# Optimization experiments

Measured on AMD Instinct MI355X. Metric: run time of the kernel, lower is better.

## Reference

```python
import jax, jax.numpy as jnp
import numpy as np

HIDDEN = 512
HEADS = 8
HEAD_DIM = HIDDEN // HEADS
N = 262144
G = 1024
LN_EPS = 1e-5
EPS = 1e-8


def setup_inputs() -> dict:
    key = jax.random.key(0)
    ks = jax.random.split(key, 4)
    x = jax.random.normal(ks[0], (N, HIDDEN), dtype=jnp.float32)
    batch = jnp.sort(jax.random.randint(ks[1], (N,), 0, G, dtype=jnp.int32))
    gamma = jnp.ones((HIDDEN,), jnp.float32)
    beta = jnp.zeros((HIDDEN,), jnp.float32)
    W1 = jax.random.normal(ks[2], (HIDDEN, HIDDEN // 2), dtype=jnp.float32) * (HIDDEN ** -0.5)
    b1 = jnp.zeros((HIDDEN // 2,), jnp.float32)
    W2 = jax.random.normal(ks[3], (HIDDEN // 2, HEADS), dtype=jnp.float32) * ((HIDDEN // 2) ** -0.5)
    b2 = jnp.zeros((HEADS,), jnp.float32)
    return {"x": x, "batch": batch, "gamma": gamma, "beta": beta,
            "W1": W1, "b1": b1, "W2": W2, "b2": b2, "num_graphs": G}


def reference(x, batch, gamma, beta, W1, b1, W2, b2, num_graphs):
    n = x.shape[0]
    # LayerNorm over feature dim
    mu = jnp.mean(x, axis=-1, keepdims=True)
    var = jnp.mean(jnp.square(x - mu), axis=-1, keepdims=True)
    x_norm = (x - mu) * jax.lax.rsqrt(var + LN_EPS) * gamma + beta
    # attention MLP -> per-head logits [N, HEADS]
    h = jax.nn.silu(x_norm @ W1 + b1)
    logits = h @ W2 + b2
    # segment softmax per head (all heads vectorized)
    seg_max = jax.ops.segment_max(logits, batch, num_segments=num_graphs)  # [G, HEADS]
    seg_max = jnp.where(jnp.isfinite(seg_max), seg_max, 0.0)  # guard empty segments
    ex = jnp.exp(logits - seg_max[batch])
    denom = jax.ops.segment_sum(ex, batch, num_segments=num_graphs)  # [G, HEADS]
    denom = jnp.where(denom > 0, denom, 1.0)
    weights = ex / denom[batch]  # [N, HEADS]
    # entropy regularizer
    entropy = -jnp.sum(weights * jnp.log(weights + EPS), axis=0) / num_graphs
    mean_entropy = jnp.mean(entropy)
    # per-head weighted features, flattened back, scatter-sum per graph
    x_split = x.reshape(n, HEADS, HEAD_DIM)
    x_weighted = (x_split * weights[:, :, None]).reshape(n, HIDDEN)
    graph_z = jax.ops.segment_sum(x_weighted, batch, num_segments=num_graphs)  # [G, HIDDEN]
    return graph_z, weights, mean_entropy
```

## Files before the change

kernel.cpp:

```cpp
#include <hip/hip_runtime.h>

#define N_ROWS 262144
#define HID 512
#define HHALF 256
#define HEADS 8
#define GNUM 1024
#define LN_EPS 1e-5f
#define POOL_ROWS 128

typedef __bf16 bf16x8 __attribute__((ext_vector_type(8)));
typedef float f32x4 __attribute__((ext_vector_type(4)));

__global__ void k_prep(const float* __restrict__ W1, __bf16* __restrict__ w1t,
                       float* __restrict__ ent, float* __restrict__ graph_z) {
    int tid = blockIdx.x * 256 + threadIdx.x;
    if (tid == 0) *ent = 0.f;
    ((float4*)graph_z)[tid] = make_float4(0.f, 0.f, 0.f, 0.f);
    if (tid < HID * HHALF) {
        int n = tid >> 9;
        int k = tid & 511;
        w1t[n * HID + k] = (__bf16)W1[k * HHALF + n];
    }
}

__global__ void k_seg(const int* __restrict__ batch, int* __restrict__ seg) {
    int g = blockIdx.x * 256 + threadIdx.x;
    if (g > GNUM) return;
    int lo = 0, hi = N_ROWS;
    while (lo < hi) {
        int mid = (lo + hi) >> 1;
        if (batch[mid] < g) lo = mid + 1; else hi = mid;
    }
    seg[g] = lo;
}

__global__ __launch_bounds__(256) void k_stats(const float* __restrict__ x,
                                               float2* __restrict__ stats) {
    int wid = threadIdx.x >> 6, lane = threadIdx.x & 63;
    int row = blockIdx.x * 4 + wid;
    const float* xr = x + (size_t)row * HID + lane * 8;
    float4 a = *(const float4*)xr;
    float4 b = *(const float4*)(xr + 4);
    float s = a.x + a.y + a.z + a.w + b.x + b.y + b.z + b.w;
    float q = a.x*a.x + a.y*a.y + a.z*a.z + a.w*a.w
            + b.x*b.x + b.y*b.y + b.z*b.z + b.w*b.w;
    #pragma unroll
    for (int m = 1; m < 64; m <<= 1) {
        s += __shfl_xor(s, m);
        q += __shfl_xor(q, m);
    }
    if (lane == 0) {
        float mu = s * (1.f / HID);
        float var = q * (1.f / HID) - mu * mu;
        stats[row] = make_float2(mu, rsqrtf(var + LN_EPS));
    }
}

__device__ inline bf16x8 make_af(const float* xp, const float* gp, const float* bp,
                                 float rstd, float nmr) {
    float4 xa = *(const float4*)xp;
    float4 xb = *(const float4*)(xp + 4);
    float4 ga = *(const float4*)gp;
    float4 gb = *(const float4*)(gp + 4);
    float4 ba = *(const float4*)bp;
    float4 bb = *(const float4*)(bp + 4);
    float xs[8] = {xa.x, xa.y, xa.z, xa.w, xb.x, xb.y, xb.z, xb.w};
    float gs[8] = {ga.x, ga.y, ga.z, ga.w, gb.x, gb.y, gb.z, gb.w};
    float bs[8] = {ba.x, ba.y, ba.z, ba.w, bb.x, bb.y, bb.z, bb.w};
    bf16x8 r;
    #pragma unroll
    for (int j = 0; j < 8; ++j)
        r[j] = (__bf16)fmaf(fmaf(xs[j], rstd, nmr), gs[j], bs[j]);
    return r;
}

__global__ __launch_bounds__(256) void k_gemm(
    const float* __restrict__ x, const float2* __restrict__ stats,
    const float* __restrict__ gamma, const float* __restrict__ beta,
    const __bf16* __restrict__ w1t, const float* __restrict__ b1,
    const float* __restrict__ W2, const float* __restrict__ b2,
    float* __restrict__ logits)
{
    __shared__ __align__(16) __bf16 ldsb[256 * 72];
    const int tid = threadIdx.x;
    const int wid = tid >> 6, lane = tid & 63;
    const int q = lane >> 4, c = lane & 15;
    const int rowbase = blockIdx.x * 64 + wid * 16;

    f32x4 acc[16];
    #pragma unroll
    for (int t = 0; t < 16; ++t) acc[t] = (f32x4)0.f;

    const int arow = rowbase + c;
    float2 st = stats[arow];
    const float rstd = st.y;
    const float nmr = -st.x * st.y;
    const float* xrow = x + (size_t)arow * HID;

    const int nrow = tid >> 3, seg = tid & 7;

    for (int s8 = 0; s8 < 8; ++s8) {
        const int k0 = s8 * 64;
        __syncthreads();
        #pragma unroll
        for (int it = 0; it < 8; ++it) {
            int n = nrow + it * 32;
            *(uint4*)(ldsb + n * 72 + seg * 8) =
                *(const uint4*)(w1t + n * HID + k0 + seg * 8);
        }
        __syncthreads();

        bf16x8 af0 = make_af(xrow + k0 + q * 8, gamma + k0 + q * 8, beta + k0 + q * 8,
                             rstd, nmr);
        bf16x8 af1 = make_af(xrow + k0 + 32 + q * 8, gamma + k0 + 32 + q * 8,
                             beta + k0 + 32 + q * 8, rstd, nmr);
        #pragma unroll
        for (int t = 0; t < 16; ++t) {
            int n = t * 16 + c;
            bf16x8 bf0 = *(const bf16x8*)(ldsb + n * 72 + q * 8);
            bf16x8 bf1 = *(const bf16x8*)(ldsb + n * 72 + 32 + q * 8);
            acc[t] = __builtin_amdgcn_mfma_f32_16x16x32_bf16(af0, bf0, acc[t], 0, 0, 0);
            acc[t] = __builtin_amdgcn_mfma_f32_16x16x32_bf16(af1, bf1, acc[t], 0, 0, 0);
        }
    }

    float lp[4][8];
    #pragma unroll
    for (int r = 0; r < 4; ++r)
        #pragma unroll
        for (int hd = 0; hd < 8; ++hd) lp[r][hd] = 0.f;

    #pragma unroll
    for (int t = 0; t < 16; ++t) {
        int n = t * 16 + c;
        float b1v = b1[n];
        float4 w2a = *(const float4*)(W2 + n * 8);
        float4 w2b = *(const float4*)(W2 + n * 8 + 4);
        #pragma unroll
        for (int r = 0; r < 4; ++r) {
            float v = acc[t][r] + b1v;
            float h = v / (1.f + __expf(-v));
            lp[r][0] = fmaf(h, w2a.x, lp[r][0]);
            lp[r][1] = fmaf(h, w2a.y, lp[r][1]);
            lp[r][2] = fmaf(h, w2a.z, lp[r][2]);
            lp[r][3] = fmaf(h, w2a.w, lp[r][3]);
            lp[r][4] = fmaf(h, w2b.x, lp[r][4]);
            lp[r][5] = fmaf(h, w2b.y, lp[r][5]);
            lp[r][6] = fmaf(h, w2b.z, lp[r][6]);
            lp[r][7] = fmaf(h, w2b.w, lp[r][7]);
        }
    }
    #pragma unroll
    for (int m = 1; m < 16; m <<= 1)
        #pragma unroll
        for (int r = 0; r < 4; ++r)
            #pragma unroll
            for (int hd = 0; hd < 8; ++hd)
                lp[r][hd] += __shfl_xor(lp[r][hd], m);

    if (c == 0) {
        float4 b2a = *(const float4*)b2;
        float4 b2b = *(const float4*)(b2 + 4);
        #pragma unroll
        for (int r = 0; r < 4; ++r) {
            int orow = rowbase + q * 4 + r;
            float4 o0 = {lp[r][0] + b2a.x, lp[r][1] + b2a.y,
                         lp[r][2] + b2a.z, lp[r][3] + b2a.w};
            float4 o1 = {lp[r][4] + b2b.x, lp[r][5] + b2b.y,
                         lp[r][6] + b2b.z, lp[r][7] + b2b.w};
            *(float4*)(logits + (size_t)orow * 8) = o0;
            *(float4*)(logits + (size_t)orow * 8 + 4) = o1;
        }
    }
}

__global__ __launch_bounds__(256) void k_smax(
    const float* __restrict__ logits, const int* __restrict__ seg,
    float* __restrict__ smaxt, float* __restrict__ sinvt)
{
    const int g = blockIdx.x;
    const int tid = threadIdx.x;
    const int s = seg[g], e = seg[g + 1];
    __shared__ float red[4][8];
    __shared__ float smx[8];
    const int wid = tid >> 6, lane = tid & 63;

    if (e <= s) {
        if (tid < 8) { smaxt[g * 8 + tid] = 0.f; sinvt[g * 8 + tid] = 1.f; }
        return;
    }
    float mx[8];
    #pragma unroll
    for (int h = 0; h < 8; ++h) mx[h] = -1e30f;
    for (int i = s + tid; i < e; i += 256) {
        float4 l0 = *(const float4*)(logits + (size_t)i * 8);
        float4 l1 = *(const float4*)(logits + (size_t)i * 8 + 4);
        mx[0] = fmaxf(mx[0], l0.x); mx[1] = fmaxf(mx[1], l0.y);
        mx[2] = fmaxf(mx[2], l0.z); mx[3] = fmaxf(mx[3], l0.w);
        mx[4] = fmaxf(mx[4], l1.x); mx[5] = fmaxf(mx[5], l1.y);
        mx[6] = fmaxf(mx[6], l1.z); mx[7] = fmaxf(mx[7], l1.w);
    }
    #pragma unroll
    for (int m = 1; m < 64; m <<= 1)
        #pragma unroll
        for (int h = 0; h < 8; ++h) mx[h] = fmaxf(mx[h], __shfl_xor(mx[h], m));
    if (lane == 0) {
        #pragma unroll
        for (int h = 0; h < 8; ++h) red[wid][h] = mx[h];
    }
    __syncthreads();
    if (tid < 8)
        smx[tid] = fmaxf(fmaxf(red[0][tid], red[1][tid]),
                         fmaxf(red[2][tid], red[3][tid]));
    __syncthreads();
    float sm[8];
    #pragma unroll
    for (int h = 0; h < 8; ++h) sm[h] = smx[h];
    float su[8] = {0, 0, 0, 0, 0, 0, 0, 0};
    for (int i = s + tid; i < e; i += 256) {
        float4 l0 = *(const float4*)(logits + (size_t)i * 8);
        float4 l1 = *(const float4*)(logits + (size_t)i * 8 + 4);
        su[0] += __expf(l0.x - sm[0]); su[1] += __expf(l0.y - sm[1]);
        su[2] += __expf(l0.z - sm[2]); su[3] += __expf(l0.w - sm[3]);
        su[4] += __expf(l1.x - sm[4]); su[5] += __expf(l1.y - sm[5]);
        su[6] += __expf(l1.z - sm[6]); su[7] += __expf(l1.w - sm[7]);
    }
    #pragma unroll
    for (int m = 1; m < 64; m <<= 1)
        #pragma unroll
        for (int h = 0; h < 8; ++h) su[h] += __shfl_xor(su[h], m);
    if (lane == 0) {
        #pragma unroll
        for (int h = 0; h < 8; ++h) red[wid][h] = su[h];
    }
    __syncthreads();
    if (tid < 8) {
        float d = red[0][tid] + red[1][tid] + red[2][tid] + red[3][tid];
        smaxt[g * 8 + tid] = smx[tid];
        sinvt[g * 8 + tid] = 1.f / (d > 0.f ? d : 1.f);
    }
}

__global__ __launch_bounds__(256) void k_wts(
    const float* __restrict__ logits, const int* __restrict__ batch,
    const float* __restrict__ smaxt, const float* __restrict__ sinvt,
    float* __restrict__ weights, float* __restrict__ ent)
{
    const int tid = threadIdx.x;
    const int i0 = blockIdx.x * 256;
    const int h = tid & 7;
    float e = 0.f;
    #pragma unroll
    for (int it = 0; it < 8; ++it) {
        int i = i0 + (tid >> 3) + it * 32;
        int g = batch[i];
        float l = logits[(size_t)i * 8 + h];
        float w = __expf(l - smaxt[g * 8 + h]) * sinvt[g * 8 + h];
        weights[(size_t)i * 8 + h] = w;
        e += w * __logf(w + 1e-8f);
    }
    #pragma unroll
    for (int m = 1; m < 64; m <<= 1) e += __shfl_xor(e, m);
    __shared__ float red[4];
    if ((tid & 63) == 0) red[tid >> 6] = e;
    __syncthreads();
    if (tid == 0)
        atomicAdd(ent, (red[0] + red[1] + red[2] + red[3]) * (-1.f / (GNUM * 8.f)));
}

__global__ __launch_bounds__(256) void k_pool2(
    const float* __restrict__ x, const int* __restrict__ batch,
    const float* __restrict__ weights, float* __restrict__ graph_z)
{
    const int tid = threadIdx.x;
    const int r0 = blockIdx.x * POOL_ROWS;
    const int h = tid >> 5;
    const int f = tid * 2;
    float a0 = 0.f, a1 = 0.f;
    int gcur = batch[r0];
    const int gend = batch[r0 + POOL_ROWS - 1];

    if (gcur == gend) {
        #pragma unroll 4
        for (int r = 0; r < POOL_ROWS; ++r) {
            const size_t i = (size_t)(r0 + r);
            float2 xv = *(const float2*)(x + i * HID + f);
            float w = weights[i * 8 + h];
            a0 = fmaf(xv.x, w, a0);
            a1 = fmaf(xv.y, w, a1);
        }
        atomicAdd(graph_z + (size_t)gcur * HID + f, a0);
        atomicAdd(graph_z + (size_t)gcur * HID + f + 1, a1);
    } else {
        for (int r = 0; r < POOL_ROWS; ++r) {
            const int i = r0 + r;
            const int g = batch[i];
            if (g != gcur) {
                atomicAdd(graph_z + (size_t)gcur * HID + f, a0);
                atomicAdd(graph_z + (size_t)gcur * HID + f + 1, a1);
                a0 = 0.f; a1 = 0.f; gcur = g;
            }
            float2 xv = *(const float2*)(x + (size_t)i * HID + f);
            float w = weights[(size_t)i * 8 + h];
            a0 = fmaf(xv.x, w, a0);
            a1 = fmaf(xv.y, w, a1);
        }
        atomicAdd(graph_z + (size_t)gcur * HID + f, a0);
        atomicAdd(graph_z + (size_t)gcur * HID + f + 1, a1);
    }
}

extern "C" void kernel_launch(void* const* d_in, const int* in_sizes, int n_in,
                              void* d_out, int out_size, void* d_ws, size_t ws_size,
                              hipStream_t stream)
{
    const float* x     = (const float*)d_in[0];
    const int*   batch = (const int*)d_in[1];
    const float* gamma = (const float*)d_in[2];
    const float* beta  = (const float*)d_in[3];
    const float* W1    = (const float*)d_in[4];
    const float* b1    = (const float*)d_in[5];
    const float* W2    = (const float*)d_in[6];
    const float* b2    = (const float*)d_in[7];

    char* ws = (char*)d_ws;
    float2* stats  = (float2*)ws;
    float*  logits = (float*)(ws + (size_t)2 * 1024 * 1024);
    __bf16* w1t    = (__bf16*)(ws + (size_t)10 * 1024 * 1024);
    int*    seg    = (int*)(ws + (size_t)10 * 1024 * 1024 + 256 * 1024);
    float*  smaxt  = (float*)(ws + (size_t)10 * 1024 * 1024 + 512 * 1024);
    float*  sinvt  = (float*)(ws + (size_t)10 * 1024 * 1024 + 576 * 1024);

    float* out     = (float*)d_out;
    float* graph_z = out;
    float* weights = out + (size_t)GNUM * HID;
    float* ent     = out + (size_t)GNUM * HID + (size_t)N_ROWS * HEADS;

    k_prep <<<512, 256, 0, stream>>>(W1, w1t, ent, graph_z);
    k_seg  <<<5, 256, 0, stream>>>(batch, seg);
    k_stats<<<N_ROWS / 4, 256, 0, stream>>>(x, stats);
    k_gemm <<<N_ROWS / 64, 256, 0, stream>>>(x, stats, gamma, beta, w1t, b1, W2, b2, logits);
    k_smax <<<GNUM, 256, 0, stream>>>(logits, seg, smaxt, sinvt);
    k_wts  <<<N_ROWS / 256, 256, 0, stream>>>(logits, batch, smaxt, sinvt, weights, ent);
    k_pool2<<<N_ROWS / POOL_ROWS, 256, 0, stream>>>(x, batch, weights, graph_z);
}
```

Measured before the change: 1.098 ms.

## Fold LayerNorm into GEMM epilogue and drop separate stats pass

Folds gamma into the bf16 W1 copy and precomputes the column sums gamma·W1 and beta·W1, so the GEMM runs on raw x and applies mean/rstd as a per-row affine correction in the epilogue. Row statistics are now computed inside the GEMM kernel from the x fragments it already loads, which removes the k_stats kernel and its extra full read of x (512 MB). The A fragments for all of K are held in registers (8x2 bf16x8), which raises register pressure and may lower occupancy. Rounding raw x to bf16 before normalization changes numerics slightly, and the column sums use atomics.

```diff
diff --git a/kernel.cpp b/kernel.cpp
--- a/kernel.cpp
+++ b/kernel.cpp
@@ -11,16 +11,34 @@
 typedef __bf16 bf16x8 __attribute__((ext_vector_type(8)));
 typedef float f32x4 __attribute__((ext_vector_type(4)));
 
-__global__ void k_prep(const float* __restrict__ W1, __bf16* __restrict__ w1t,
-                       float* __restrict__ ent, float* __restrict__ graph_z) {
+__global__ void k_prep(const float* __restrict__ W1, const float* __restrict__ gamma,
+                       __bf16* __restrict__ w1t, float* __restrict__ ent,
+                       float* __restrict__ graph_z, float* __restrict__ G1,
+                       float* __restrict__ BB) {
     int tid = blockIdx.x * 256 + threadIdx.x;
     if (tid == 0) *ent = 0.f;
+    if (blockIdx.x == 0) { G1[threadIdx.x] = 0.f; BB[threadIdx.x] = 0.f; }
     ((float4*)graph_z)[tid] = make_float4(0.f, 0.f, 0.f, 0.f);
-    if (tid < HID * HHALF) {
-        int n = tid >> 9;
-        int k = tid & 511;
-        w1t[n * HID + k] = (__bf16)W1[k * HHALF + n];
-    }
+    int n = tid >> 9;
+    int k = tid & 511;
+    w1t[n * HID + k] = (__bf16)(gamma[k] * W1[k * HHALF + n]);
+}
+
+__global__ void k_cols(const float* __restrict__ W1, const float* __restrict__ gamma,
+                       const float* __restrict__ beta, float* __restrict__ G1,
+                       float* __restrict__ BB) {
+    int n = threadIdx.x;
+    int k0 = blockIdx.x * 64;
+    float g = 0.f, b = 0.f;
+    #pragma unroll
+    for (int kk = 0; kk < 64; ++kk) {
+        int k = k0 + kk;
+        float w = W1[(size_t)k * HHALF + n];
+        g = fmaf(gamma[k], w, g);
+        b = fmaf(beta[k], w, b);
+    }
+    atomicAdd(G1 + n, g);
+    atomicAdd(BB + n, b);
 }
 
 __global__ void k_seg(const int* __restrict__ batch, int* __restrict__ seg) {
@@ -34,50 +52,17 @@
     seg[g] = lo;
 }
 
-__global__ __launch_bounds__(256) void k_stats(const float* __restrict__ x,
-                                               float2* __restrict__ stats) {
-    int wid = threadIdx.x >> 6, lane = threadIdx.x & 63;
-    int row = blockIdx.x * 4 + wid;
-    const float* xr = x + (size_t)row * HID + lane * 8;
-    float4 a = *(const float4*)xr;
-    float4 b = *(const float4*)(xr + 4);
-    float s = a.x + a.y + a.z + a.w + b.x + b.y + b.z + b.w;
-    float q = a.x*a.x + a.y*a.y + a.z*a.z + a.w*a.w
-            + b.x*b.x + b.y*b.y + b.z*b.z + b.w*b.w;
-    #pragma unroll
-    for (int m = 1; m < 64; m <<= 1) {
-        s += __shfl_xor(s, m);
-        q += __shfl_xor(q, m);
-    }
-    if (lane == 0) {
-        float mu = s * (1.f / HID);
-        float var = q * (1.f / HID) - mu * mu;
-        stats[row] = make_float2(mu, rsqrtf(var + LN_EPS));
-    }
-}
-
-__device__ inline bf16x8 make_af(const float* xp, const float* gp, const float* bp,
-                                 float rstd, float nmr) {
-    float4 xa = *(const float4*)xp;
-    float4 xb = *(const float4*)(xp + 4);
-    float4 ga = *(const float4*)gp;
-    float4 gb = *(const float4*)(gp + 4);
-    float4 ba = *(const float4*)bp;
-    float4 bb = *(const float4*)(bp + 4);
-    float xs[8] = {xa.x, xa.y, xa.z, xa.w, xb.x, xb.y, xb.z, xb.w};
-    float gs[8] = {ga.x, ga.y, ga.z, ga.w, gb.x, gb.y, gb.z, gb.w};
-    float bs[8] = {ba.x, ba.y, ba.z, ba.w, bb.x, bb.y, bb.z, bb.w};
+__device__ inline bf16x8 pack8(float4 a, float4 b) {
     bf16x8 r;
-    #pragma unroll
-    for (int j = 0; j < 8; ++j)
-        r[j] = (__bf16)fmaf(fmaf(xs[j], rstd, nmr), gs[j], bs[j]);
+    r[0] = (__bf16)a.x; r[1] = (__bf16)a.y; r[2] = (__bf16)a.z; r[3] = (__bf16)a.w;
+    r[4] = (__bf16)b.x; r[5] = (__bf16)b.y; r[6] = (__bf16)b.z; r[7] = (__bf16)b.w;
     return r;
 }
 
 __global__ __launch_bounds__(256) void k_gemm(
-    const float* __restrict__ x, const float2* __restrict__ stats,
-    const float* __restrict__ gamma, const float* __restrict__ beta,
+    const float* __restrict__ x,
     const __bf16* __restrict__ w1t, const float* __restrict__ b1,
+    const float* __restrict__ G1, const float* __restrict__ BB,
     const float* __restrict__ W2, const float* __restrict__ b2,
     float* __restrict__ logits)
 {
@@ -86,42 +71,69 @@
     const int wid = tid >> 6, lane = tid & 63;
     const int q = lane >> 4, c = lane & 15;
     const int rowbase = blockIdx.x * 64 + wid * 16;
+    const float* xrow = x + (size_t)(rowbase + c) * HID;
+
+    bf16x8 af[8][2];
+    float s = 0.f, qq = 0.f;
+    #pragma unroll
+    for (int s8 = 0; s8 < 8; ++s8) {
+        float4 a = *(const float4*)(xrow + s8 * 64 + q * 8);
+        float4 b = *(const float4*)(xrow + s8 * 64 + q * 8 + 4);
+        float4 d = *(const float4*)(xrow + s8 * 64 + 32 + q * 8);
+        float4 e = *(const float4*)(xrow + s8 * 64 + 32 + q * 8 + 4);
+        s += a.x + a.y + a.z + a.w + b.x + b.y + b.z + b.w
+           + d.x + d.y + d.z + d.w + e.x + e.y + e.z + e.w;
+        qq = fmaf(a.x, a.x, qq); qq = fmaf(a.y, a.y, qq);
+        qq = fmaf(a.z, a.z, qq); qq = fmaf(a.w, a.w, qq);
+        qq = fmaf(b.x, b.x, qq); qq = fmaf(b.y, b.y, qq);
+        qq = fmaf(b.z, b.z, qq); qq = fmaf(b.w, b.w, qq);
+        qq = fmaf(d.x, d.x, qq); qq = fmaf(d.y, d.y, qq);
+        qq = fmaf(d.z, d.z, qq); qq = fmaf(d.w, d.w, qq);
+        qq = fmaf(e.x, e.x, qq); qq = fmaf(e.y, e.y, qq);
+        qq = fmaf(e.z, e.z, qq); qq = fmaf(e.w, e.w, qq);
+        af[s8][0] = pack8(a, b);
+        af[s8][1] = pack8(d, e);
+    }
+    s  += __shfl_xor(s, 16);  s  += __shfl_xor(s, 32);
+    qq += __shfl_xor(qq, 16); qq += __shfl_xor(qq, 32);
+    const float mu = s * (1.f / HID);
+    const float var = qq * (1.f / HID) - mu * mu;
+    const float rstd = rsqrtf(var + LN_EPS);
+    const float nmr = -mu * rstd;
 
     f32x4 acc[16];
     #pragma unroll
     for (int t = 0; t < 16; ++t) acc[t] = (f32x4)0.f;
 
-    const int arow = rowbase + c;
-    float2 st = stats[arow];
-    const float rstd = st.y;
-    const float nmr = -st.x * st.y;
-    const float* xrow = x + (size_t)arow * HID;
-
-    const int nrow = tid >> 3, seg = tid & 7;
-
+    const int nrow = tid >> 3, sg = tid & 7;
+
+    #pragma unroll
     for (int s8 = 0; s8 < 8; ++s8) {
         const int k0 = s8 * 64;
         __syncthreads();
         #pragma unroll
         for (int it = 0; it < 8; ++it) {
             int n = nrow + it * 32;
-            *(uint4*)(ldsb + n * 72 + seg * 8) =
-                *(const uint4*)(w1t + n * HID + k0 + seg * 8);
+            *(uint4*)(ldsb + n * 72 + sg * 8) =
+                *(const uint4*)(w1t + n * HID + k0 + sg * 8);
         }
         __syncthreads();
-
-        bf16x8 af0 = make_af(xrow + k0 + q * 8, gamma + k0 + q * 8, beta + k0 + q * 8,
-                             rstd, nmr);
-        bf16x8 af1 = make_af(xrow + k0 + 32 + q * 8, gamma + k0 + 32 + q * 8,
-                             beta + k0 + 32 + q * 8, rstd, nmr);
         #pragma unroll
         for (int t = 0; t < 16; ++t) {
             int n = t * 16 + c;
             bf16x8 bf0 = *(const bf16x8*)(ldsb + n * 72 + q * 8);
             bf16x8 bf1 = *(const bf16x8*)(ldsb + n * 72 + 32 + q * 8);
-            acc[t] = __builtin_amdgcn_mfma_f32_16x16x32_bf16(af0, bf0, acc[t], 0, 0, 0);
-            acc[t] = __builtin_amdgcn_mfma_f32_16x16x32_bf16(af1, bf1, acc[t], 0, 0, 0);
-        }
+            acc[t] = __builtin_amdgcn_mfma_f32_16x16x32_bf16(af[s8][0], bf0, acc[t], 0, 0, 0);
+            acc[t] = __builtin_amdgcn_mfma_f32_16x16x32_bf16(af[s8][1], bf1, acc[t], 0, 0, 0);
+        }
+    }
+
+    float rstd_r[4], nmr_r[4];
+    #pragma unroll
+    for (int r = 0; r < 4; ++r) {
+        int src = (lane & 48) | (q * 4 + r);
+        rstd_r[r] = __shfl(rstd, src);
+        nmr_r[r]  = __shfl(nmr, src);
     }
 
     float lp[4][8];
@@ -133,12 +145,13 @@
     #pragma unroll
     for (int t = 0; t < 16; ++t) {
         int n = t * 16 + c;
-        float b1v = b1[n];
+        float g1v = G1[n];
+        float cbv = BB[n] + b1[n];
         float4 w2a = *(const float4*)(W2 + n * 8);
         float4 w2b = *(const float4*)(W2 + n * 8 + 4);
         #pragma unroll
         for (int r = 0; r < 4; ++r) {
-            float v = acc[t][r] + b1v;
+            float v = fmaf(rstd_r[r], acc[t][r], fmaf(nmr_r[r], g1v, cbv));
             float h = v / (1.f + __expf(-v));
             lp[r][0] = fmaf(h, w2a.x, lp[r][0]);
             lp[r][1] = fmaf(h, w2a.y, lp[r][1]);
@@ -324,22 +337,23 @@
     const float* b2    = (const float*)d_in[7];
 
     char* ws = (char*)d_ws;
-    float2* stats  = (float2*)ws;
-    float*  logits = (float*)(ws + (size_t)2 * 1024 * 1024);
-    __bf16* w1t    = (__bf16*)(ws + (size_t)10 * 1024 * 1024);
-    int*    seg    = (int*)(ws + (size_t)10 * 1024 * 1024 + 256 * 1024);
-    float*  smaxt  = (float*)(ws + (size_t)10 * 1024 * 1024 + 512 * 1024);
-    float*  sinvt  = (float*)(ws + (size_t)10 * 1024 * 1024 + 576 * 1024);
+    float*  logits = (float*)ws;
+    __bf16* w1t    = (__bf16*)(ws + (size_t)8 * 1024 * 1024);
+    int*    seg    = (int*)(ws + (size_t)8 * 1024 * 1024 + 256 * 1024);
+    float*  G1     = (float*)(ws + (size_t)8 * 1024 * 1024 + 272 * 1024);
+    float*  BB     = (float*)(ws + (size_t)8 * 1024 * 1024 + 276 * 1024);
+    float*  smaxt  = (float*)(ws + (size_t)8 * 1024 * 1024 + 288 * 1024);
+    float*  sinvt  = (float*)(ws + (size_t)8 * 1024 * 1024 + 320 * 1024);
 
     float* out     = (float*)d_out;
     float* graph_z = out;
     float* weights = out + (size_t)GNUM * HID;
     float* ent     = out + (size_t)GNUM * HID + (size_t)N_ROWS * HEADS;
 
-    k_prep <<<512, 256, 0, stream>>>(W1, w1t, ent, graph_z);
+    k_prep <<<512, 256, 0, stream>>>(W1, gamma, w1t, ent, graph_z, G1, BB);
+    k_cols <<<8, 256, 0, stream>>>(W1, gamma, beta, G1, BB);
     k_seg  <<<5, 256, 0, stream>>>(batch, seg);
-    k_stats<<<N_ROWS / 4, 256, 0, stream>>>(x, stats);
-    k_gemm <<<N_ROWS / 64, 256, 0, stream>>>(x, stats, gamma, beta, w1t, b1, W2, b2, logits);
+    k_gemm <<<N_ROWS / 64, 256, 0, stream>>>(x, w1t, b1, G1, BB, W2, b2, logits);
     k_smax <<<GNUM, 256, 0, stream>>>(logits, seg, smaxt, sinvt);
     k_wts  <<<N_ROWS / 256, 256, 0, stream>>>(logits, batch, smaxt, sinvt, weights, ent);
     k_pool2<<<N_ROWS / POOL_ROWS, 256, 0, stream>>>(x, batch, weights, graph_z);
```

New measurement: 1.012 ms. 7.9% less time.
